# Kernel tuning notes

Measured on AMD Instinct MI355X. Metric: run time of the kernel, lower is better.

The kernel has to match this reference:

```python
import jax, jax.numpy as jnp
import numpy as np

N_NODES = 50000
N_EDGES = 800000
H = 128
D = 128
N_LAYERS = 4
N_GRAPHS = 128
NODE_VOCAB = 32
EDGE_VOCAB = 8
BN_EPS = 1e-5


def _bn(h, g, b):
    # BatchNorm1d, training-mode statistics (biased variance), as in the torch module
    m = h.mean(axis=0)
    v = ((h - m) ** 2).mean(axis=0)
    return (h - m) * jax.lax.rsqrt(v + BN_EPS) * g + b


def _gine(x, src, dst, e, eps_l):
    # GINEConv: message = ReLU(x_src + edge_attr), sum-aggregate at dst
    msg = jax.nn.relu(x[src] + e)                      # [E, H]
    aggr = jax.ops.segment_sum(msg, dst, num_segments=N_NODES)
    return (1.0 + eps_l) * x + aggr


def _forward(x_ids, edge_index, batch, edge_attr,
             node_emb, edge_emb, eps,
             init_W1, init_b1, init_g1, init_be1, init_W2, init_b2, init_g2, init_be2,
             mp_W1, mp_g1, mp_be1, mp_W2, mp_g2, mp_be2,
             l1_W1, l1_g1, l1_b1, l1_W2, l1_g2, l1_b2,
             l2_W1, l2_g1, l2_b1, l2_W2, l2_g2, l2_b2,
             fin_W):
    src, dst = edge_index[0], edge_index[1]
    x = node_emb[x_ids]                                # [N, H]
    e = edge_emb[edge_attr]                            # [E, H]
    # initialization conv (Linear layers WITH bias)
    h = _gine(x, src, dst, e, eps[0])
    h = jax.nn.relu(_bn(h @ init_W1 + init_b1, init_g1, init_be1))
    x = jax.nn.relu(_bn(h @ init_W2 + init_b2, init_g2, init_be2))
    # message-passing layers (Linear layers WITHOUT bias)
    for i in range(N_LAYERS):
        h = _gine(x, src, dst, e, eps[1 + i])
        h = jax.nn.relu(_bn(h @ mp_W1[i], mp_g1[i], mp_be1[i]))
        x = jax.nn.relu(_bn(h @ mp_W2[i], mp_g2[i], mp_be2[i]))
    # readout: global_add_pool
    g = jax.ops.segment_sum(x, batch, num_segments=N_GRAPHS)   # [G, H]
    # lin1 (outer F.relu is idempotent; dropout = identity in eval)
    h = jax.nn.relu(_bn(g @ l1_W1, l1_g1, l1_b1))
    h = jax.nn.relu(_bn(h @ l1_W2, l1_g2, l1_b2))
    # lin2
    h = jax.nn.relu(_bn(h @ l2_W1, l2_g1, l2_b1))
    h = jax.nn.relu(_bn(h @ l2_W2, l2_g2, l2_b2))
    return h @ fin_W                                   # [G, 1]


def setup_inputs() -> dict:
    key = jax.random.key(0)
    ks = jax.random.split(key, 20)
    s = 1.0 / np.sqrt(H)
    rn = lambda k, shp, sc: jax.random.normal(k, shp, dtype=jnp.float32) * sc
    return {
        "x_ids": jax.random.randint(ks[0], (N_NODES,), 0, NODE_VOCAB),
        "edge_index": jax.random.randint(ks[1], (2, N_EDGES), 0, N_NODES),
        "batch": jnp.sort(jax.random.randint(ks[2], (N_NODES,), 0, N_GRAPHS)),
        "edge_attr": jax.random.randint(ks[14], (N_EDGES,), 0, EDGE_VOCAB),
        "node_emb": rn(ks[3], (NODE_VOCAB, H), 0.05),
        "edge_emb": rn(ks[4], (EDGE_VOCAB, H), 0.05),
        "eps": jnp.zeros((N_LAYERS + 1,), jnp.float32),
        "init_W1": rn(ks[5], (H, D), s), "init_b1": jnp.zeros((D,)),
        "init_g1": jnp.ones((D,)), "init_be1": jnp.zeros((D,)),
        "init_W2": rn(ks[6], (D, H), s), "init_b2": jnp.zeros((H,)),
        "init_g2": jnp.ones((H,)), "init_be2": jnp.zeros((H,)),
        "mp_W1": rn(ks[7], (N_LAYERS, H, D), s),
        "mp_g1": jnp.ones((N_LAYERS, D)), "mp_be1": jnp.zeros((N_LAYERS, D)),
        "mp_W2": rn(ks[8], (N_LAYERS, D, H), s),
        "mp_g2": jnp.ones((N_LAYERS, H)), "mp_be2": jnp.zeros((N_LAYERS, H)),
        "l1_W1": rn(ks[9], (H, D), s), "l1_g1": jnp.ones((D,)), "l1_b1": jnp.zeros((D,)),
        "l1_W2": rn(ks[10], (D, D), s), "l1_g2": jnp.ones((D,)), "l1_b2": jnp.zeros((D,)),
        "l2_W1": rn(ks[11], (D, D), s), "l2_g1": jnp.ones((D,)), "l2_b1": jnp.zeros((D,)),
        "l2_W2": rn(ks[12], (D, H), s), "l2_g2": jnp.ones((H,)), "l2_b2": jnp.zeros((H,)),
        "fin_W": rn(ks[13], (H, 1), s),
    }


def reference(x_ids, edge_index, batch, edge_attr,
              node_emb, edge_emb, eps,
              init_W1, init_b1, init_g1, init_be1, init_W2, init_b2, init_g2, init_be2,
              mp_W1, mp_g1, mp_be1, mp_W2, mp_g2, mp_be2,
              l1_W1, l1_g1, l1_b1, l1_W2, l1_g2, l1_b2,
              l2_W1, l2_g1, l2_b1, l2_W2, l2_g2, l2_b2,
              fin_W):
    return _forward(x_ids, edge_index, batch, edge_attr,
                    node_emb, edge_emb, eps,
                    init_W1, init_b1, init_g1, init_be1, init_W2, init_b2, init_g2, init_be2,
                    mp_W1, mp_g1, mp_be1, mp_W2, mp_g2, mp_be2,
                    l1_W1, l1_g1, l1_b1, l1_W2, l1_g2, l1_b2,
                    l2_W1, l2_g1, l2_b1, l2_W2, l2_g2, l2_b2,
                    fin_W)
```

## Files before the change

### kernel.cpp

```cpp
#include <hip/hip_runtime.h>

#define NN 50000
#define NE 800000
#define NG 128
#define HD 128
#define NL 4
#define BN_EPS 1e-5f
#define REP 32
#define WP 136
#define NB 392
#define EPB 4096

typedef __attribute__((ext_vector_type(8))) short bf16x8;
typedef __attribute__((ext_vector_type(4))) float f32x4;

__device__ __forceinline__ unsigned short f2bf(float f) {
    unsigned u = __float_as_uint(f);
    u += 0x7FFFu + ((u >> 16) & 1u);
    return (unsigned short)(u >> 16);
}
__device__ __forceinline__ float bfval(unsigned short h) { return __uint_as_float((unsigned)h << 16); }
__device__ __forceinline__ float bflo(unsigned u) { return __uint_as_float(u << 16); }
__device__ __forceinline__ float bfhi(unsigned u) { return __uint_as_float(u & 0xFFFF0000u); }

__device__ __forceinline__ void split2(float a, float b, unsigned& hi, unsigned& lo) {
    unsigned ua = __float_as_uint(a), ub = __float_as_uint(b);
    hi = (ua >> 16) | (ub & 0xFFFF0000u);
    float ra = a - __uint_as_float(ua & 0xFFFF0000u);
    float rb = b - __uint_as_float(ub & 0xFFFF0000u);
    lo = (unsigned)f2bf(ra) | ((unsigned)f2bf(rb) << 16);
}
__device__ __forceinline__ unsigned pack2(float a, float b) {
    return (unsigned)f2bf(a) | ((unsigned)f2bf(b) << 16);
}

__device__ __forceinline__ void bn_pre(const float* SQbase,
                                       const float* gam, const float* bet,
                                       float inv_cnt, int t, float* scs, float* shs) {
    if (gam == nullptr) { scs[t] = 1.f; shs[t] = 0.f; return; }
    float s = 0.f, q = 0.f;
#pragma unroll
    for (int r = 0; r < REP; r++) {
        s += SQbase[r * 256 + t];
        q += SQbase[r * 256 + 128 + t];
    }
    float m = s * inv_cnt;
    float var = fmaxf(fmaf(q, inv_cnt, -m * m), 0.f);
    float inv = rsqrtf(var + BN_EPS);
    float sc = gam[t] * inv;
    scs[t] = sc;
    shs[t] = fmaf(-m, sc, bet[t]);
}

__global__ __launch_bounds__(256) void setup_kernel(const int* __restrict__ ids,
                                                    const float* __restrict__ emb,
                                                    unsigned short* __restrict__ Yb,
                                                    const float* __restrict__ iw1,
                                                    const float* __restrict__ iw2,
                                                    const float* __restrict__ mw1,
                                                    const float* __restrict__ mw2,
                                                    const float* __restrict__ hw1,
                                                    const float* __restrict__ hw2,
                                                    const float* __restrict__ hw3,
                                                    const float* __restrict__ hw4,
                                                    unsigned short* __restrict__ Wh,
                                                    unsigned short* __restrict__ Wl,
                                                    const int* __restrict__ dst,
                                                    int* __restrict__ deg) {
    int b = blockIdx.x, t = threadIdx.x;
    if (b < 3125) {
        int i = b * 256 + t;
        if (i < NN * 16) {
            int node = i >> 4, g = i & 15;
            int id = ids[node];
            const float* p = emb + (size_t)id * HD + 8 * g;
            float4 a = *(const float4*)p;
            float4 bb = *(const float4*)(p + 4);
            uint4 o;
            o.x = pack2(a.x, a.y); o.y = pack2(a.z, a.w);
            o.z = pack2(bb.x, bb.y); o.w = pack2(bb.z, bb.w);
            *(uint4*)(Yb + (size_t)node * HD + 8 * g) = o;
        }
    } else if (b < 4021) {
        int i = (b - 3125) * 256 + t;
        if (i < 229376) {
            int seg = i >> 14, loc = i & 16383;
            float v;
            if (seg == 0)       v = iw1[loc];
            else if (seg == 1)  v = iw2[loc];
            else if (seg < 6)   v = mw1[(seg - 2) * 16384 + loc];
            else if (seg < 10)  v = mw2[(seg - 6) * 16384 + loc];
            else if (seg == 10) v = hw1[loc];
            else if (seg == 11) v = hw2[loc];
            else if (seg == 12) v = hw3[loc];
            else                v = hw4[loc];
            int k = loc >> 7, n = loc & 127;
            unsigned short h = f2bf(v);
            float r = v - bfval(h);
            Wh[seg * 16384 + n * 128 + k] = h;
            Wl[seg * 16384 + n * 128 + k] = f2bf(r);
        }
    } else {
        int e = (b - 4021) * 256 + t;
        if (e < NE) atomicAdd(&deg[dst[e]], 1);
    }
}

__global__ __launch_bounds__(256) void ybn_kernel(const float* __restrict__ X,
                                                  const float* __restrict__ SQin,
                                                  const float* __restrict__ gam,
                                                  const float* __restrict__ bet,
                                                  unsigned short* __restrict__ Yb) {
    __shared__ float scs[HD], shs[HD];
    int t = threadIdx.x;
    if (t < HD) bn_pre(SQin, gam, bet, 1.f / NN, t, scs, shs);
    __syncthreads();
    int c8 = (t & 15) * 8;
    float4 s0 = *(const float4*)&scs[c8], s1 = *(const float4*)&scs[c8 + 4];
    float4 h0 = *(const float4*)&shs[c8], h1 = *(const float4*)&shs[c8 + 4];
#pragma unroll
    for (int ch = 0; ch < 4; ch++) {
        int row = blockIdx.x * 64 + ch * 16 + (t >> 4);
        if (row < NN) {
            const float* p = X + (size_t)row * HD + c8;
            float4 v0 = *(const float4*)p;
            float4 v1 = *(const float4*)(p + 4);
            float f0 = fmaxf(fmaf(v0.x, s0.x, h0.x), 0.f), f1 = fmaxf(fmaf(v0.y, s0.y, h0.y), 0.f);
            float f2 = fmaxf(fmaf(v0.z, s0.z, h0.z), 0.f), f3 = fmaxf(fmaf(v0.w, s0.w, h0.w), 0.f);
            float f4 = fmaxf(fmaf(v1.x, s1.x, h1.x), 0.f), f5 = fmaxf(fmaf(v1.y, s1.y, h1.y), 0.f);
            float f6 = fmaxf(fmaf(v1.z, s1.z, h1.z), 0.f), f7 = fmaxf(fmaf(v1.w, s1.w, h1.w), 0.f);
            uint4 o;
            o.x = pack2(f0, f1); o.y = pack2(f2, f3);
            o.z = pack2(f4, f5); o.w = pack2(f6, f7);
            *(uint4*)(Yb + (size_t)row * HD + c8) = o;
        }
    }
}

__global__ __launch_bounds__(1024) void scan1_kernel(const int* __restrict__ deg,
                                                     int* __restrict__ rowptr,
                                                     int* __restrict__ blockSum) {
    __shared__ int s[1024];
    int b = blockIdx.x, t = threadIdx.x;
    int i = b * 1024 + t;
    int v = (i < NN) ? deg[i] : 0;
    s[t] = v;
    __syncthreads();
    for (int off = 1; off < 1024; off <<= 1) {
        int u = (t >= off) ? s[t - off] : 0;
        __syncthreads();
        s[t] += u;
        __syncthreads();
    }
    if (i < NN) rowptr[i] = s[t] - v;
    if (t == 1023) blockSum[b] = s[1023];
}

__global__ __launch_bounds__(1024) void scan3_kernel(int* __restrict__ rowptr,
                                                     int* __restrict__ cursor,
                                                     const int* __restrict__ blockSum,
                                                     int* __restrict__ bucketCursor,
                                                     int nblocks) {
    __shared__ int sOff, sTot;
    int b = blockIdx.x, t = threadIdx.x;
    if (t < 64) {
        int orig = (t < nblocks) ? blockSum[t] : 0;
        int v = orig;
        for (int off = 1; off < 64; off <<= 1) {
            int u = __shfl_up(v, off, 64);
            if (t >= off) v += u;
        }
        if (t == b) sOff = v - orig;
        if (t == nblocks - 1) sTot = v;
    }
    __syncthreads();
    int i = b * 1024 + t;
    if (i < NN) {
        int r = rowptr[i] + sOff;
        rowptr[i] = r;
        cursor[i] = r;
        if ((i & 127) == 0) bucketCursor[i >> 7] = r;
    }
    if (b == nblocks - 1 && t == 0) rowptr[NN] = sTot;
}

__global__ __launch_bounds__(256) void bin_kernel(const int* __restrict__ src,
                                                  const int* __restrict__ dst,
                                                  const int* __restrict__ attr,
                                                  int* __restrict__ bucketCursor,
                                                  uint2* __restrict__ ebuf) {
    __shared__ int cnt[512];
    __shared__ int sc[512], sc2[512];
    __shared__ int base[512];
    __shared__ int garr[NB];
    __shared__ int wof[NB];
    __shared__ uint2 stage[EPB];
    int t = threadIdx.x;
    int e0 = blockIdx.x * EPB;
    for (int i = t; i < 512; i += 256) cnt[i] = 0;
    __syncthreads();
    int myb[16]; unsigned myv[16]; int myd[16];
#pragma unroll
    for (int j = 0; j < 16; j++) {
        int e = e0 + t + j * 256;
        if (e < NE) {
            int d = dst[e];
            myd[j] = d;
            myv[j] = (unsigned)src[e] | ((unsigned)attr[e] << 16);
            myb[j] = d >> 7;
            atomicAdd(&cnt[myb[j]], 1);
        } else myb[j] = -1;
    }
    __syncthreads();
    for (int k = t; k < 512; k += 256) sc[k] = cnt[k];
    __syncthreads();
    int* sp = sc; int* dp = sc2;
    for (int off = 1; off < 512; off <<= 1) {
        for (int k = t; k < 512; k += 256) dp[k] = sp[k] + (k >= off ? sp[k - off] : 0);
        __syncthreads();
        int* tmp = sp; sp = dp; dp = tmp;
    }
    for (int k = t; k < 512; k += 256) base[k] = sp[k] - cnt[k];
    int total = sp[511];
    __syncthreads();
    for (int b = t; b < NB; b += 256) {
        wof[b] = 0;
        if (cnt[b] > 0) garr[b] = atomicAdd(&bucketCursor[b], cnt[b]);
    }
    __syncthreads();
#pragma unroll
    for (int j = 0; j < 16; j++) {
        if (myb[j] >= 0) {
            int slot = base[myb[j]] + atomicAdd(&wof[myb[j]], 1);
            stage[slot] = make_uint2(myv[j], (unsigned)myd[j]);
        }
    }
    __syncthreads();
    for (int i = t; i < total; i += 256) {
        uint2 u = stage[i];
        int b = (int)(u.y >> 7);
        ebuf[garr[b] + (i - base[b])] = u;
    }
}

__global__ __launch_bounds__(256) void place_kernel(const uint2* __restrict__ ebuf,
                                                    const int* __restrict__ rowptr,
                                                    int* __restrict__ cursor,
                                                    unsigned* __restrict__ csr) {
    int b = blockIdx.x;
    int n0 = b * 128;
    int n1 = n0 + 128; if (n1 > NN) n1 = NN;
    int es = rowptr[n0], ee = rowptr[n1];
    for (int i = es + threadIdx.x; i < ee; i += 256) {
        uint2 u = ebuf[i];
        int pos = atomicAdd(&cursor[u.y], 1);
        csr[pos] = u.x;
    }
}

__device__ __forceinline__ void gine_acc(const unsigned short* __restrict__ Yb,
                                         const float* __restrict__ elds,
                                         unsigned p, int cq, float mask, float* a) {
    uint4 q = *(const uint4*)(Yb + (size_t)(p & 0xFFFFu) * HD + 8 * cq);
    const float* ep = elds + (p >> 16) * HD + 8 * cq;
    float4 e0 = *(const float4*)ep;
    float4 e1 = *(const float4*)(ep + 4);
    a[0] += mask * fmaxf(bflo(q.x) + e0.x, 0.f);
    a[1] += mask * fmaxf(bfhi(q.x) + e0.y, 0.f);
    a[2] += mask * fmaxf(bflo(q.y) + e0.z, 0.f);
    a[3] += mask * fmaxf(bfhi(q.y) + e0.w, 0.f);
    a[4] += mask * fmaxf(bflo(q.z) + e1.x, 0.f);
    a[5] += mask * fmaxf(bfhi(q.z) + e1.y, 0.f);
    a[6] += mask * fmaxf(bflo(q.w) + e1.z, 0.f);
    a[7] += mask * fmaxf(bfhi(q.w) + e1.w, 0.f);
}

__global__ __launch_bounds__(256) void conv_kernel(const unsigned short* __restrict__ Yb,
                                                   const int* __restrict__ rowptr,
                                                   const unsigned* __restrict__ csr,
                                                   const float* __restrict__ edge_emb,
                                                   const float* __restrict__ eps, int layer,
                                                   unsigned short* __restrict__ Ah,
                                                   unsigned short* __restrict__ Al) {
    __shared__ float elds[8 * HD];
    int t = threadIdx.x;
    ((float4*)elds)[t] = ((const float4*)edge_emb)[t];
    __syncthreads();
    int wave = t >> 6, lane = t & 63;
    int node = blockIdx.x * 4 + wave;
    if (node >= NN) return;
    int sub = lane >> 4, cq = lane & 15;
    int lo = rowptr[node], hi = rowptr[node + 1];
    float a[8];
#pragma unroll
    for (int i = 0; i < 8; i++) a[i] = 0.f;
    for (int base = lo; base < hi; base += 64) {
        unsigned pl = 0;
        int cnt = hi - base; if (cnt > 64) cnt = 64;
        if (base + lane < hi) pl = csr[base + lane];
        int j = 0;
        for (; j + 16 <= cnt; j += 16) {
            unsigned pa = __shfl(pl, j + sub, 64);
            unsigned pb = __shfl(pl, j + 4 + sub, 64);
            unsigned pc = __shfl(pl, j + 8 + sub, 64);
            unsigned pd = __shfl(pl, j + 12 + sub, 64);
            gine_acc(Yb, elds, pa, cq, 1.f, a);
            gine_acc(Yb, elds, pb, cq, 1.f, a);
            gine_acc(Yb, elds, pc, cq, 1.f, a);
            gine_acc(Yb, elds, pd, cq, 1.f, a);
        }
        for (; j + 8 <= cnt; j += 8) {
            unsigned pa = __shfl(pl, j + sub, 64);
            unsigned pb = __shfl(pl, j + 4 + sub, 64);
            gine_acc(Yb, elds, pa, cq, 1.f, a);
            gine_acc(Yb, elds, pb, cq, 1.f, a);
        }
        for (; j < cnt; j += 4) {
            int je = j + sub;
            bool val = (je < cnt);
            unsigned p = __shfl(pl, val ? je : j, 64);
            gine_acc(Yb, elds, p, cq, val ? 1.f : 0.f, a);
        }
    }
#pragma unroll
    for (int i = 0; i < 8; i++) {
        a[i] += __shfl_xor(a[i], 16, 64);
        a[i] += __shfl_xor(a[i], 32, 64);
    }
    if (sub == 0) {
        float g = 1.f + eps[layer];
        uint4 q = *(const uint4*)(Yb + (size_t)node * HD + 8 * cq);
        float o0 = fmaf(g, bflo(q.x), a[0]), o1 = fmaf(g, bfhi(q.x), a[1]);
        float o2 = fmaf(g, bflo(q.y), a[2]), o3 = fmaf(g, bfhi(q.y), a[3]);
        float o4 = fmaf(g, bflo(q.z), a[4]), o5 = fmaf(g, bfhi(q.z), a[5]);
        float o6 = fmaf(g, bflo(q.w), a[6]), o7 = fmaf(g, bfhi(q.w), a[7]);
        uint4 H, L;
        split2(o0, o1, H.x, L.x);
        split2(o2, o3, H.y, L.y);
        split2(o4, o5, H.z, L.z);
        split2(o6, o7, H.w, L.w);
        *(uint4*)(Ah + (size_t)node * HD + 8 * cq) = H;
        *(uint4*)(Al + (size_t)node * HD + 8 * cq) = L;
    }
}

__global__ __launch_bounds__(512) void mm_mfma_pre(const unsigned short* __restrict__ Ah,
                                                   const unsigned short* __restrict__ Al,
                                                   const unsigned short* __restrict__ Wh,
                                                   const unsigned short* __restrict__ Wl,
                                                   const float* __restrict__ bias,
                                                   float* __restrict__ out,
                                                   float* __restrict__ SQout) {
    __shared__ unsigned short WhS[128 * WP];
    __shared__ unsigned short WlS[128 * WP];
    int t = threadIdx.x;
    int rowblk = blockIdx.x;
#pragma unroll
    for (int i = 0; i < 4; i++) {
        int idx = t + i * 512;
        int col = idx >> 4, kk = (idx & 15) * 8;
        *(uint4*)(WhS + col * WP + kk) = *(const uint4*)(Wh + (size_t)col * HD + kk);
        *(uint4*)(WlS + col * WP + kk) = *(const uint4*)(Wl + (size_t)col * HD + kk);
    }
    __syncthreads();
    int w = t >> 6, lane = t & 63;
    int quad = lane >> 4, nl = lane & 15;
    int row0 = rowblk * 128 + w * 16;
    int rA0 = row0 + nl;
    bool ok0 = rA0 < NN;
    f32x4 acc[8];
#pragma unroll
    for (int i = 0; i < 8; i++) acc[i] = (f32x4){0.f, 0.f, 0.f, 0.f};
#pragma unroll
    for (int kc = 0; kc < 4; kc++) {
        int k0 = kc * 32 + quad * 8;
        bf16x8 a0h = ok0 ? *(const bf16x8*)(Ah + (size_t)rA0 * HD + k0) : (bf16x8)0;
        bf16x8 a0l = ok0 ? *(const bf16x8*)(Al + (size_t)rA0 * HD + k0) : (bf16x8)0;
#pragma unroll
        for (int c = 0; c < 8; c++) {
            int wof = (c * 16 + nl) * WP + k0;
            bf16x8 bh = *(const bf16x8*)(WhS + wof);
            bf16x8 bl = *(const bf16x8*)(WlS + wof);
            acc[c] = __builtin_amdgcn_mfma_f32_16x16x32_bf16(a0h, bh, acc[c], 0, 0, 0);
            acc[c] = __builtin_amdgcn_mfma_f32_16x16x32_bf16(a0l, bh, acc[c], 0, 0, 0);
            acc[c] = __builtin_amdgcn_mfma_f32_16x16x32_bf16(a0h, bl, acc[c], 0, 0, 0);
        }
    }
    int rep = (blockIdx.x & (REP - 1)) * 256;
    int baserow = row0 + quad * 4;
    if (rowblk * 128 + 128 <= NN) {
#pragma unroll
        for (int c = 0; c < 8; c++) {
            int col = c * 16 + nl;
            float bv = bias ? bias[col] : 0.f;
            f32x4 v = acc[c];
            float s = 0.f, qq = 0.f;
#pragma unroll
            for (int r = 0; r < 4; r++) {
                float val = v[r] + bv;
                out[(size_t)(baserow + r) * HD + col] = val;
                s += val;
                qq += val * val;
            }
            s += __shfl_xor(s, 16, 64);  s += __shfl_xor(s, 32, 64);
            qq += __shfl_xor(qq, 16, 64); qq += __shfl_xor(qq, 32, 64);
            if (quad == 0) {
                atomicAdd(&SQout[rep + col], s);
                atomicAdd(&SQout[rep + 128 + col], qq);
            }
        }
    } else {
#pragma unroll
        for (int c = 0; c < 8; c++) {
            int col = c * 16 + nl;
            float bv = bias ? bias[col] : 0.f;
            f32x4 v = acc[c];
            float s = 0.f, qq = 0.f;
#pragma unroll
            for (int r = 0; r < 4; r++) {
                int grow = baserow + r;
                float val = v[r] + bv;
                if (grow < NN) {
                    out[(size_t)grow * HD + col] = val;
                    s += val;
                    qq += val * val;
                }
            }
            s += __shfl_xor(s, 16, 64);  s += __shfl_xor(s, 32, 64);
            qq += __shfl_xor(qq, 16, 64); qq += __shfl_xor(qq, 32, 64);
            if (quad == 0) {
                atomicAdd(&SQout[rep + col], s);
                atomicAdd(&SQout[rep + 128 + col], qq);
            }
        }
    }
}

__global__ __launch_bounds__(512) void mm_mfma_act(const float* __restrict__ A,
                                                   const unsigned short* __restrict__ Wh,
                                                   const unsigned short* __restrict__ Wl,
                                                   const float* __restrict__ bias,
                                                   const float* __restrict__ SQin,
                                                   const float* __restrict__ gam,
                                                   const float* __restrict__ bet,
                                                   float* __restrict__ out,
                                                   float* __restrict__ SQout) {
    __shared__ unsigned short WhS[128 * WP];
    __shared__ unsigned short WlS[128 * WP];
    __shared__ float scs[HD], shs[HD];
    int t = threadIdx.x;
    int rowblk = blockIdx.x;
    if (t < HD) bn_pre(SQin, gam, bet, 1.f / NN, t, scs, shs);
#pragma unroll
    for (int i = 0; i < 4; i++) {
        int idx = t + i * 512;
        int col = idx >> 4, kk = (idx & 15) * 8;
        *(uint4*)(WhS + col * WP + kk) = *(const uint4*)(Wh + (size_t)col * HD + kk);
        *(uint4*)(WlS + col * WP + kk) = *(const uint4*)(Wl + (size_t)col * HD + kk);
    }
    __syncthreads();
    int w = t >> 6, lane = t & 63;
    int quad = lane >> 4, nl = lane & 15;
    int row0 = rowblk * 128 + w * 16;
    int rA0 = row0 + nl;
    bool ok0 = rA0 < NN;
    f32x4 acc[8];
#pragma unroll
    for (int i = 0; i < 8; i++) acc[i] = (f32x4){0.f, 0.f, 0.f, 0.f};
#pragma unroll
    for (int kc = 0; kc < 4; kc++) {
        int k0 = kc * 32 + quad * 8;
        float4 s0 = *(const float4*)&scs[k0], s1 = *(const float4*)&scs[k0 + 4];
        float4 t0 = *(const float4*)&shs[k0], t1 = *(const float4*)&shs[k0 + 4];
        bf16x8 a0h, a0l;
        {
            float4 v0 = ok0 ? *(const float4*)(A + (size_t)rA0 * HD + k0) : make_float4(0, 0, 0, 0);
            float4 v1 = ok0 ? *(const float4*)(A + (size_t)rA0 * HD + k0 + 4) : make_float4(0, 0, 0, 0);
            float f0 = fmaxf(fmaf(v0.x, s0.x, t0.x), 0.f), f1 = fmaxf(fmaf(v0.y, s0.y, t0.y), 0.f);
            float f2 = fmaxf(fmaf(v0.z, s0.z, t0.z), 0.f), f3 = fmaxf(fmaf(v0.w, s0.w, t0.w), 0.f);
            float f4 = fmaxf(fmaf(v1.x, s1.x, t1.x), 0.f), f5 = fmaxf(fmaf(v1.y, s1.y, t1.y), 0.f);
            float f6 = fmaxf(fmaf(v1.z, s1.z, t1.z), 0.f), f7 = fmaxf(fmaf(v1.w, s1.w, t1.w), 0.f);
            if (!ok0) { f0 = f1 = f2 = f3 = f4 = f5 = f6 = f7 = 0.f; }
            unsigned h0, h1, h2, h3, l0, l1, l2, l3;
            split2(f0, f1, h0, l0); split2(f2, f3, h1, l1);
            split2(f4, f5, h2, l2); split2(f6, f7, h3, l3);
            a0h = __builtin_bit_cast(bf16x8, make_uint4(h0, h1, h2, h3));
            a0l = __builtin_bit_cast(bf16x8, make_uint4(l0, l1, l2, l3));
        }
#pragma unroll
        for (int c = 0; c < 8; c++) {
            int wof = (c * 16 + nl) * WP + k0;
            bf16x8 bh = *(const bf16x8*)(WhS + wof);
            bf16x8 bl = *(const bf16x8*)(WlS + wof);
            acc[c] = __builtin_amdgcn_mfma_f32_16x16x32_bf16(a0h, bh, acc[c], 0, 0, 0);
            acc[c] = __builtin_amdgcn_mfma_f32_16x16x32_bf16(a0l, bh, acc[c], 0, 0, 0);
            acc[c] = __builtin_amdgcn_mfma_f32_16x16x32_bf16(a0h, bl, acc[c], 0, 0, 0);
        }
    }
    int rep = (blockIdx.x & (REP - 1)) * 256;
    int baserow = row0 + quad * 4;
    if (rowblk * 128 + 128 <= NN) {
#pragma unroll
        for (int c = 0; c < 8; c++) {
            int col = c * 16 + nl;
            float bv = bias ? bias[col] : 0.f;
            f32x4 v = acc[c];
            float s = 0.f, qq = 0.f;
#pragma unroll
            for (int r = 0; r < 4; r++) {
                float val = v[r] + bv;
                out[(size_t)(baserow + r) * HD + col] = val;
                s += val;
                qq += val * val;
            }
            s += __shfl_xor(s, 16, 64);  s += __shfl_xor(s, 32, 64);
            qq += __shfl_xor(qq, 16, 64); qq += __shfl_xor(qq, 32, 64);
            if (quad == 0) {
                atomicAdd(&SQout[rep + col], s);
                atomicAdd(&SQout[rep + 128 + col], qq);
            }
        }
    } else {
#pragma unroll
        for (int c = 0; c < 8; c++) {
            int col = c * 16 + nl;
            float bv = bias ? bias[col] : 0.f;
            f32x4 v = acc[c];
            float s = 0.f, qq = 0.f;
#pragma unroll
            for (int r = 0; r < 4; r++) {
                int grow = baserow + r;
                float val = v[r] + bv;
                if (grow < NN) {
                    out[(size_t)grow * HD + col] = val;
                    s += val;
                    qq += val * val;
                }
            }
            s += __shfl_xor(s, 16, 64);  s += __shfl_xor(s, 32, 64);
            qq += __shfl_xor(qq, 16, 64); qq += __shfl_xor(qq, 32, 64);
            if (quad == 0) {
                atomicAdd(&SQout[rep + col], s);
                atomicAdd(&SQout[rep + 128 + col], qq);
            }
        }
    }
}

__global__ __launch_bounds__(256) void readout_kernel(const float* __restrict__ x,
                                                      const int* __restrict__ batch,
                                                      const float* __restrict__ SQin,
                                                      const float* __restrict__ gam,
                                                      const float* __restrict__ bet,
                                                      float* __restrict__ gout) {
    __shared__ int bat[256];
    __shared__ float scs[HD], shs[HD];
    int t = threadIdx.x;
    int rq = t >> 5, cq = t & 31;
    int r0 = blockIdx.x * 256;
    int i = r0 + t;
    bat[t] = (i < NN) ? batch[i] : -1;
    if (t < HD) bn_pre(SQin, gam, bet, 1.f / NN, t, scs, shs);
    __syncthreads();
    float4 s4 = *(const float4*)&scs[4 * cq];
    float4 h4 = *(const float4*)&shs[4 * cq];
    float4 acc = make_float4(0.f, 0.f, 0.f, 0.f);
    int gcur = -1;
    for (int j = rq; j < 256; j += 8) {
        int r = r0 + j;
        if (r >= NN) break;
        int g = bat[j];
        if (g != gcur) {
            if (gcur >= 0) {
                atomicAdd(&gout[(size_t)gcur * HD + 4 * cq + 0], acc.x);
                atomicAdd(&gout[(size_t)gcur * HD + 4 * cq + 1], acc.y);
                atomicAdd(&gout[(size_t)gcur * HD + 4 * cq + 2], acc.z);
                atomicAdd(&gout[(size_t)gcur * HD + 4 * cq + 3], acc.w);
            }
            acc = make_float4(0.f, 0.f, 0.f, 0.f);
            gcur = g;
        }
        float4 v = *(const float4*)(x + (size_t)r * HD + 4 * cq);
        acc.x += fmaxf(fmaf(v.x, s4.x, h4.x), 0.f);
        acc.y += fmaxf(fmaf(v.y, s4.y, h4.y), 0.f);
        acc.z += fmaxf(fmaf(v.z, s4.z, h4.z), 0.f);
        acc.w += fmaxf(fmaf(v.w, s4.w, h4.w), 0.f);
    }
    if (gcur >= 0) {
        atomicAdd(&gout[(size_t)gcur * HD + 4 * cq + 0], acc.x);
        atomicAdd(&gout[(size_t)gcur * HD + 4 * cq + 1], acc.y);
        atomicAdd(&gout[(size_t)gcur * HD + 4 * cq + 2], acc.z);
        atomicAdd(&gout[(size_t)gcur * HD + 4 * cq + 3], acc.w);
    }
}

__global__ __launch_bounds__(1024) void head_fused(const float* __restrict__ Gp,
                                                   const unsigned short* __restrict__ Whd,
                                                   const unsigned short* __restrict__ Wld,
                                                   const float* __restrict__ g0,
                                                   const float* __restrict__ b0,
                                                   const float* __restrict__ g1,
                                                   const float* __restrict__ b1,
                                                   const float* __restrict__ g2,
                                                   const float* __restrict__ b2,
                                                   const float* __restrict__ g3,
                                                   const float* __restrict__ b3,
                                                   const float* __restrict__ finW,
                                                   float* __restrict__ out) {
    const int AP = 132;
    __shared__ float A_lds[128 * AP];
    __shared__ unsigned short WhS[128 * WP];
    __shared__ unsigned short WlS[128 * WP];
    __shared__ float colS[HD], colQ[HD], scs[HD], shs[HD];
    int t = threadIdx.x;
    if (t < HD) { colS[t] = 0.f; colQ[t] = 0.f; scs[t] = 1.f; shs[t] = 0.f; }
#pragma unroll
    for (int i = 0; i < 4; i++) {
        int idx = t + i * 1024;
        int r = idx >> 5, cq = (idx & 31) * 4;
        *(float4*)&A_lds[r * AP + cq] = *(const float4*)(Gp + (size_t)r * HD + cq);
    }
    int sc_ = t >> 4;
    int sk_ = (t & 15) * 8;
    const float* gs[4] = {g0, g1, g2, g3};
    const float* bs[4] = {b0, b1, b2, b3};
    uint4 ph0 = *(const uint4*)(Whd + (size_t)sc_ * HD + sk_);
    uint4 ph1 = *(const uint4*)(Whd + (size_t)(sc_ + 64) * HD + sk_);
    uint4 pl0 = *(const uint4*)(Wld + (size_t)sc_ * HD + sk_);
    uint4 pl1 = *(const uint4*)(Wld + (size_t)(sc_ + 64) * HD + sk_);
    int w = t >> 6, lane = t & 63;
    int quad = lane >> 4, nl = lane & 15;
    int row0 = (w >> 2) * 32, col0 = (w & 3) * 32;
#pragma unroll
    for (int s = 0; s < 4; s++) {
        *(uint4*)(WhS + sc_ * WP + sk_) = ph0;
        *(uint4*)(WhS + (sc_ + 64) * WP + sk_) = ph1;
        *(uint4*)(WlS + sc_ * WP + sk_) = pl0;
        *(uint4*)(WlS + (sc_ + 64) * WP + sk_) = pl1;
        __syncthreads();
        if (s < 3) {
            const unsigned short* nh = Whd + (size_t)(s + 1) * 16384;
            const unsigned short* nl2 = Wld + (size_t)(s + 1) * 16384;
            ph0 = *(const uint4*)(nh + (size_t)sc_ * HD + sk_);
            ph1 = *(const uint4*)(nh + (size_t)(sc_ + 64) * HD + sk_);
            pl0 = *(const uint4*)(nl2 + (size_t)sc_ * HD + sk_);
            pl1 = *(const uint4*)(nl2 + (size_t)(sc_ + 64) * HD + sk_);
        }
        f32x4 acc[4];
#pragma unroll
        for (int i = 0; i < 4; i++) acc[i] = (f32x4){0.f, 0.f, 0.f, 0.f};
#pragma unroll
        for (int kc = 0; kc < 4; kc++) {
            int k0 = kc * 32 + quad * 8;
            float4 s0 = *(const float4*)&scs[k0], s1 = *(const float4*)&scs[k0 + 4];
            float4 t0 = *(const float4*)&shs[k0], t1 = *(const float4*)&shs[k0 + 4];
            bf16x8 a0h, a0l, a1h, a1l;
            {
                const float* ap = &A_lds[(row0 + nl) * AP + k0];
                float4 v0 = *(const float4*)ap;
                float4 v1 = *(const float4*)(ap + 4);
                float f0 = fmaxf(fmaf(v0.x, s0.x, t0.x), 0.f), f1 = fmaxf(fmaf(v0.y, s0.y, t0.y), 0.f);
                float f2 = fmaxf(fmaf(v0.z, s0.z, t0.z), 0.f), f3 = fmaxf(fmaf(v0.w, s0.w, t0.w), 0.f);
                float f4 = fmaxf(fmaf(v1.x, s1.x, t1.x), 0.f), f5 = fmaxf(fmaf(v1.y, s1.y, t1.y), 0.f);
                float f6 = fmaxf(fmaf(v1.z, s1.z, t1.z), 0.f), f7 = fmaxf(fmaf(v1.w, s1.w, t1.w), 0.f);
                unsigned h0, h1, h2, h3, l0, l1, l2, l3;
                split2(f0, f1, h0, l0); split2(f2, f3, h1, l1);
                split2(f4, f5, h2, l2); split2(f6, f7, h3, l3);
                a0h = __builtin_bit_cast(bf16x8, make_uint4(h0, h1, h2, h3));
                a0l = __builtin_bit_cast(bf16x8, make_uint4(l0, l1, l2, l3));
            }
            {
                const float* ap = &A_lds[(row0 + 16 + nl) * AP + k0];
                float4 v0 = *(const float4*)ap;
                float4 v1 = *(const float4*)(ap + 4);
                float f0 = fmaxf(fmaf(v0.x, s0.x, t0.x), 0.f), f1 = fmaxf(fmaf(v0.y, s0.y, t0.y), 0.f);
                float f2 = fmaxf(fmaf(v0.z, s0.z, t0.z), 0.f), f3 = fmaxf(fmaf(v0.w, s0.w, t0.w), 0.f);
                float f4 = fmaxf(fmaf(v1.x, s1.x, t1.x), 0.f), f5 = fmaxf(fmaf(v1.y, s1.y, t1.y), 0.f);
                float f6 = fmaxf(fmaf(v1.z, s1.z, t1.z), 0.f), f7 = fmaxf(fmaf(v1.w, s1.w, t1.w), 0.f);
                unsigned h0, h1, h2, h3, l0, l1, l2, l3;
                split2(f0, f1, h0, l0); split2(f2, f3, h1, l1);
                split2(f4, f5, h2, l2); split2(f6, f7, h3, l3);
                a1h = __builtin_bit_cast(bf16x8, make_uint4(h0, h1, h2, h3));
                a1l = __builtin_bit_cast(bf16x8, make_uint4(l0, l1, l2, l3));
            }
#pragma unroll
            for (int cc = 0; cc < 2; cc++) {
                int wof = (col0 + cc * 16 + nl) * WP + k0;
                bf16x8 bh = *(const bf16x8*)(WhS + wof);
                bf16x8 bl = *(const bf16x8*)(WlS + wof);
                acc[cc] = __builtin_amdgcn_mfma_f32_16x16x32_bf16(a0h, bh, acc[cc], 0, 0, 0);
                acc[cc] = __builtin_amdgcn_mfma_f32_16x16x32_bf16(a0l, bh, acc[cc], 0, 0, 0);
                acc[cc] = __builtin_amdgcn_mfma_f32_16x16x32_bf16(a0h, bl, acc[cc], 0, 0, 0);
                acc[2 + cc] = __builtin_amdgcn_mfma_f32_16x16x32_bf16(a1h, bh, acc[2 + cc], 0, 0, 0);
                acc[2 + cc] = __builtin_amdgcn_mfma_f32_16x16x32_bf16(a1l, bh, acc[2 + cc], 0, 0, 0);
                acc[2 + cc] = __builtin_amdgcn_mfma_f32_16x16x32_bf16(a1h, bl, acc[2 + cc], 0, 0, 0);
            }
        }
        __syncthreads();
#pragma unroll
        for (int h = 0; h < 2; h++) {
            int baserow = row0 + h * 16 + quad * 4;
#pragma unroll
            for (int cc = 0; cc < 2; cc++) {
                int col = col0 + cc * 16 + nl;
                f32x4 v = acc[h * 2 + cc];
                float ss = 0.f, qq = 0.f;
#pragma unroll
                for (int r = 0; r < 4; r++) {
                    float val = v[r];
                    A_lds[(baserow + r) * AP + col] = val;
                    ss += val;
                    qq += val * val;
                }
                ss += __shfl_xor(ss, 16, 64);  ss += __shfl_xor(ss, 32, 64);
                qq += __shfl_xor(qq, 16, 64);  qq += __shfl_xor(qq, 32, 64);
                if (quad == 0) {
                    atomicAdd(&colS[col], ss);
                    atomicAdd(&colQ[col], qq);
                }
            }
        }
        __syncthreads();
        if (t < HD) {
            float m = colS[t] * (1.f / NG);
            float var = fmaxf(fmaf(colQ[t], 1.f / NG, -m * m), 0.f);
            float inv = rsqrtf(var + BN_EPS);
            float sc = gs[s][t] * inv;
            scs[t] = sc;
            shs[t] = fmaf(-m, sc, bs[s][t]);
            colS[t] = 0.f;
            colQ[t] = 0.f;
        }
        __syncthreads();
    }
    int r = t >> 3, g = t & 7;
    float ssum = 0.f;
#pragma unroll
    for (int j = 0; j < 16; j++) {
        int c = g * 16 + j;
        float v = fmaxf(fmaf(A_lds[r * AP + c], scs[c], shs[c]), 0.f);
        ssum += v * finW[c];
    }
    ssum += __shfl_xor(ssum, 1, 64);
    ssum += __shfl_xor(ssum, 2, 64);
    ssum += __shfl_xor(ssum, 4, 64);
    if (g == 0) out[r] = ssum;
}

extern "C" void kernel_launch(void* const* d_in, const int* in_sizes, int n_in,
                              void* d_out, int out_size, void* d_ws, size_t ws_size,
                              hipStream_t stream) {
    const int* x_ids = (const int*)d_in[0];
    const int* edge_index = (const int*)d_in[1];
    const int* batch = (const int*)d_in[2];
    const int* edge_attr = (const int*)d_in[3];
    const float* node_emb = (const float*)d_in[4];
    const float* edge_emb = (const float*)d_in[5];
    const float* eps = (const float*)d_in[6];
    const float* init_W1 = (const float*)d_in[7];
    const float* init_b1 = (const float*)d_in[8];
    const float* init_g1 = (const float*)d_in[9];
    const float* init_be1 = (const float*)d_in[10];
    const float* init_W2 = (const float*)d_in[11];
    const float* init_b2 = (const float*)d_in[12];
    const float* init_g2 = (const float*)d_in[13];
    const float* init_be2 = (const float*)d_in[14];
    const float* mp_W1 = (const float*)d_in[15];
    const float* mp_g1 = (const float*)d_in[16];
    const float* mp_be1 = (const float*)d_in[17];
    const float* mp_W2 = (const float*)d_in[18];
    const float* mp_g2 = (const float*)d_in[19];
    const float* mp_be2 = (const float*)d_in[20];
    const float* l1_W1 = (const float*)d_in[21];
    const float* l1_g1 = (const float*)d_in[22];
    const float* l1_b1 = (const float*)d_in[23];
    const float* l1_W2 = (const float*)d_in[24];
    const float* l1_g2 = (const float*)d_in[25];
    const float* l1_b2 = (const float*)d_in[26];
    const float* l2_W1 = (const float*)d_in[27];
    const float* l2_g1 = (const float*)d_in[28];
    const float* l2_b1 = (const float*)d_in[29];
    const float* l2_W2 = (const float*)d_in[30];
    const float* l2_g2 = (const float*)d_in[31];
    const float* l2_b2 = (const float*)d_in[32];
    const float* fin_W = (const float*)d_in[33];

    const int* e_src = edge_index;
    const int* e_dst = edge_index + NE;

    const size_t STG = (size_t)REP * 256;
    float* ws = (float*)d_ws;
    float* X = ws;
    float* Bbuf = X + (size_t)NN * HD;
    unsigned short* Yb = (unsigned short*)Bbuf;
    unsigned short* Ah = (unsigned short*)(Bbuf + (size_t)NN * HD);
    unsigned short* Al = Ah + (size_t)NN * HD;
    float* SQ = (float*)(Al + (size_t)NN * HD);
    float* Gp = SQ + 14 * STG;
    int* deg = (int*)(Gp + NG * HD);
    float* Hp = (float*)(deg + 50048);
    float* Hp2 = Hp + NG * HD;
    int* rowptr = (int*)(Hp2 + NG * HD);
    int* cursor = rowptr + 50048;
    int* blockSum = cursor + 50048;
    int* blockOff = blockSum + 64;
    int* bucketCursor = blockOff + 64;
    unsigned* csr = (unsigned*)(bucketCursor + NB);
    unsigned short* Wh = (unsigned short*)(csr + NE);
    unsigned short* Wl = Wh + 229376;
    uint2* ebuf = (uint2*)(Wl + 229376);
    (void)Hp; (void)Hp2; (void)blockOff;

    const size_t zero_bytes = (14 * STG + NG * HD) * sizeof(float) + 50048 * sizeof(int);
    hipMemsetAsync(SQ, 0, zero_bytes, stream);

    const int SCAN_BLOCKS = (NN + 1023) / 1024;
    setup_kernel<<<7146, 256, 0, stream>>>(x_ids, node_emb, Yb, init_W1, init_W2, mp_W1,
                                           mp_W2, l1_W1, l1_W2, l2_W1, l2_W2,
                                           Wh, Wl, e_dst, deg);
    scan1_kernel<<<SCAN_BLOCKS, 1024, 0, stream>>>(deg, rowptr, blockSum);
    scan3_kernel<<<SCAN_BLOCKS, 1024, 0, stream>>>(rowptr, cursor, blockSum, bucketCursor,
                                                   SCAN_BLOCKS);
    bin_kernel<<<(NE + EPB - 1) / EPB, 256, 0, stream>>>(e_src, e_dst, edge_attr,
                                                         bucketCursor, ebuf);
    place_kernel<<<(NN + 127) / 128, 256, 0, stream>>>(ebuf, rowptr, cursor, csr);

    const int mfma_grid = (NN + 127) / 128;
    const int ybn_grid = (NN + 63) / 64;
    for (int i = 0; i <= NL; i++) {
        const unsigned short* Wh1 = Wh + (size_t)(i == 0 ? 0 : 2 + (i - 1)) * 16384;
        const unsigned short* Wl1 = Wl + (size_t)(i == 0 ? 0 : 2 + (i - 1)) * 16384;
        const unsigned short* Wh2 = Wh + (size_t)(i == 0 ? 1 : 6 + (i - 1)) * 16384;
        const unsigned short* Wl2 = Wl + (size_t)(i == 0 ? 1 : 6 + (i - 1)) * 16384;
        const float* b1 = (i == 0) ? init_b1 : nullptr;
        const float* b2 = (i == 0) ? init_b2 : nullptr;
        const float* g1 = (i == 0) ? init_g1 : mp_g1 + (size_t)(i - 1) * HD;
        const float* be1 = (i == 0) ? init_be1 : mp_be1 + (size_t)(i - 1) * HD;
        const float* gp = (i == 1) ? init_g2 : mp_g2 + (size_t)(i - 2) * HD;
        const float* bp = (i == 1) ? init_be2 : mp_be2 + (size_t)(i - 2) * HD;
        float* Sprev = SQ + (size_t)(2 * i - 1) * STG;
        float* S1 = SQ + (size_t)(2 * i) * STG;
        float* S2 = SQ + (size_t)(2 * i + 1) * STG;

        if (i > 0) ybn_kernel<<<ybn_grid, 256, 0, stream>>>(X, Sprev, gp, bp, Yb);
        conv_kernel<<<(NN + 3) / 4, 256, 0, stream>>>(Yb, rowptr, csr, edge_emb, eps, i, Ah, Al);
        mm_mfma_pre<<<mfma_grid, 512, 0, stream>>>(Ah, Al, Wh1, Wl1, b1, Bbuf, S1);
        mm_mfma_act<<<mfma_grid, 512, 0, stream>>>(Bbuf, Wh2, Wl2, b2, S1, g1, be1, X, S2);
    }

    float* S9 = SQ + 9 * STG;
    readout_kernel<<<(NN + 255) / 256, 256, 0, stream>>>(
        X, batch, S9, mp_g2 + 3 * HD, mp_be2 + 3 * HD, Gp);

    head_fused<<<1, 1024, 0, stream>>>(Gp, Wh + (size_t)10 * 16384, Wl + (size_t)10 * 16384,
                                       l1_g1, l1_b1, l1_g2, l1_b2,
                                       l2_g1, l2_b1, l2_g2, l2_b2,
                                       fin_W, (float*)d_out);
}
```

Before: 675.7 us.

## Fuse two MFMA GEMM kernels with an in-kernel grid barrier for BN stats

Merges the two per-layer MFMA matmul kernels into one persistent launch. A global atomic-counter barrier waits for all blocks' first-GEMM BatchNorm statistics before the second GEMM runs. This removes one kernel launch per layer and keeps the block's rows hot in cache between the GEMMs. It relies on all ~391 blocks being co-resident (launch_bounds 512,4) to avoid deadlock, and adds spin-wait overhead. The barrier counters sit inside the memset-zeroed deg region.

```diff
diff --git a/kernel.cpp b/kernel.cpp
--- a/kernel.cpp
+++ b/kernel.cpp
@@ -344,23 +344,32 @@
     }
 }
 
-__global__ __launch_bounds__(512) void mm_mfma_pre(const unsigned short* __restrict__ Ah,
+__global__ __launch_bounds__(512, 4) void mm_fused(const unsigned short* __restrict__ Ah,
                                                    const unsigned short* __restrict__ Al,
-                                                   const unsigned short* __restrict__ Wh,
-                                                   const unsigned short* __restrict__ Wl,
-                                                   const float* __restrict__ bias,
-                                                   float* __restrict__ out,
-                                                   float* __restrict__ SQout) {
+                                                   const unsigned short* __restrict__ Wh1,
+                                                   const unsigned short* __restrict__ Wl1,
+                                                   const float* __restrict__ bias1,
+                                                   const unsigned short* __restrict__ Wh2,
+                                                   const unsigned short* __restrict__ Wl2,
+                                                   const float* __restrict__ bias2,
+                                                   const float* __restrict__ gam,
+                                                   const float* __restrict__ bet,
+                                                   float* __restrict__ Bbuf,
+                                                   float* __restrict__ S1,
+                                                   float* __restrict__ X,
+                                                   float* __restrict__ S2,
+                                                   int* __restrict__ barCnt, int nblk) {
     __shared__ unsigned short WhS[128 * WP];
     __shared__ unsigned short WlS[128 * WP];
+    __shared__ float scs[HD], shs[HD];
     int t = threadIdx.x;
     int rowblk = blockIdx.x;
 #pragma unroll
     for (int i = 0; i < 4; i++) {
         int idx = t + i * 512;
         int col = idx >> 4, kk = (idx & 15) * 8;
-        *(uint4*)(WhS + col * WP + kk) = *(const uint4*)(Wh + (size_t)col * HD + kk);
-        *(uint4*)(WlS + col * WP + kk) = *(const uint4*)(Wl + (size_t)col * HD + kk);
+        *(uint4*)(WhS + col * WP + kk) = *(const uint4*)(Wh1 + (size_t)col * HD + kk);
+        *(uint4*)(WlS + col * WP + kk) = *(const uint4*)(Wl1 + (size_t)col * HD + kk);
     }
     __syncthreads();
     int w = t >> 6, lane = t & 63;
@@ -368,180 +377,170 @@
     int row0 = rowblk * 128 + w * 16;
     int rA0 = row0 + nl;
     bool ok0 = rA0 < NN;
-    f32x4 acc[8];
-#pragma unroll
-    for (int i = 0; i < 8; i++) acc[i] = (f32x4){0.f, 0.f, 0.f, 0.f};
-#pragma unroll
-    for (int kc = 0; kc < 4; kc++) {
-        int k0 = kc * 32 + quad * 8;
-        bf16x8 a0h = ok0 ? *(const bf16x8*)(Ah + (size_t)rA0 * HD + k0) : (bf16x8)0;
-        bf16x8 a0l = ok0 ? *(const bf16x8*)(Al + (size_t)rA0 * HD + k0) : (bf16x8)0;
-#pragma unroll
-        for (int c = 0; c < 8; c++) {
-            int wof = (c * 16 + nl) * WP + k0;
-            bf16x8 bh = *(const bf16x8*)(WhS + wof);
-            bf16x8 bl = *(const bf16x8*)(WlS + wof);
-            acc[c] = __builtin_amdgcn_mfma_f32_16x16x32_bf16(a0h, bh, acc[c], 0, 0, 0);
-            acc[c] = __builtin_amdgcn_mfma_f32_16x16x32_bf16(a0l, bh, acc[c], 0, 0, 0);
-            acc[c] = __builtin_amdgcn_mfma_f32_16x16x32_bf16(a0h, bl, acc[c], 0, 0, 0);
-        }
-    }
-    int rep = (blockIdx.x & (REP - 1)) * 256;
+    bool fullblk = (rowblk * 128 + 128 <= NN);
+    int rep = (rowblk & (REP - 1)) * 256;
     int baserow = row0 + quad * 4;
-    if (rowblk * 128 + 128 <= NN) {
-#pragma unroll
-        for (int c = 0; c < 8; c++) {
-            int col = c * 16 + nl;
-            float bv = bias ? bias[col] : 0.f;
-            f32x4 v = acc[c];
-            float s = 0.f, qq = 0.f;
-#pragma unroll
-            for (int r = 0; r < 4; r++) {
-                float val = v[r] + bv;
-                out[(size_t)(baserow + r) * HD + col] = val;
-                s += val;
-                qq += val * val;
-            }
-            s += __shfl_xor(s, 16, 64);  s += __shfl_xor(s, 32, 64);
-            qq += __shfl_xor(qq, 16, 64); qq += __shfl_xor(qq, 32, 64);
-            if (quad == 0) {
-                atomicAdd(&SQout[rep + col], s);
-                atomicAdd(&SQout[rep + 128 + col], qq);
-            }
-        }
-    } else {
-#pragma unroll
-        for (int c = 0; c < 8; c++) {
-            int col = c * 16 + nl;
-            float bv = bias ? bias[col] : 0.f;
-            f32x4 v = acc[c];
-            float s = 0.f, qq = 0.f;
-#pragma unroll
-            for (int r = 0; r < 4; r++) {
-                int grow = baserow + r;
-                float val = v[r] + bv;
-                if (grow < NN) {
-                    out[(size_t)grow * HD + col] = val;
+    {
+        f32x4 acc[8];
+#pragma unroll
+        for (int i = 0; i < 8; i++) acc[i] = (f32x4){0.f, 0.f, 0.f, 0.f};
+#pragma unroll
+        for (int kc = 0; kc < 4; kc++) {
+            int k0 = kc * 32 + quad * 8;
+            bf16x8 a0h = ok0 ? *(const bf16x8*)(Ah + (size_t)rA0 * HD + k0) : (bf16x8)0;
+            bf16x8 a0l = ok0 ? *(const bf16x8*)(Al + (size_t)rA0 * HD + k0) : (bf16x8)0;
+#pragma unroll
+            for (int c = 0; c < 8; c++) {
+                int wof = (c * 16 + nl) * WP + k0;
+                bf16x8 bh = *(const bf16x8*)(WhS + wof);
+                bf16x8 bl = *(const bf16x8*)(WlS + wof);
+                acc[c] = __builtin_amdgcn_mfma_f32_16x16x32_bf16(a0h, bh, acc[c], 0, 0, 0);
+                acc[c] = __builtin_amdgcn_mfma_f32_16x16x32_bf16(a0l, bh, acc[c], 0, 0, 0);
+                acc[c] = __builtin_amdgcn_mfma_f32_16x16x32_bf16(a0h, bl, acc[c], 0, 0, 0);
+            }
+        }
+        if (fullblk) {
+#pragma unroll
+            for (int c = 0; c < 8; c++) {
+                int col = c * 16 + nl;
+                float bv = bias1 ? bias1[col] : 0.f;
+                f32x4 v = acc[c];
+                float s = 0.f, qq = 0.f;
+#pragma unroll
+                for (int r = 0; r < 4; r++) {
+                    float val = v[r] + bv;
+                    Bbuf[(size_t)(baserow + r) * HD + col] = val;
                     s += val;
                     qq += val * val;
                 }
-            }
-            s += __shfl_xor(s, 16, 64);  s += __shfl_xor(s, 32, 64);
-            qq += __shfl_xor(qq, 16, 64); qq += __shfl_xor(qq, 32, 64);
-            if (quad == 0) {
-                atomicAdd(&SQout[rep + col], s);
-                atomicAdd(&SQout[rep + 128 + col], qq);
-            }
-        }
-    }
-}
-
-__global__ __launch_bounds__(512) void mm_mfma_act(const float* __restrict__ A,
-                                                   const unsigned short* __restrict__ Wh,
-                                                   const unsigned short* __restrict__ Wl,
-                                                   const float* __restrict__ bias,
-                                                   const float* __restrict__ SQin,
-                                                   const float* __restrict__ gam,
-                                                   const float* __restrict__ bet,
-                                                   float* __restrict__ out,
-                                                   float* __restrict__ SQout) {
-    __shared__ unsigned short WhS[128 * WP];
-    __shared__ unsigned short WlS[128 * WP];
-    __shared__ float scs[HD], shs[HD];
-    int t = threadIdx.x;
-    int rowblk = blockIdx.x;
-    if (t < HD) bn_pre(SQin, gam, bet, 1.f / NN, t, scs, shs);
+                s += __shfl_xor(s, 16, 64);  s += __shfl_xor(s, 32, 64);
+                qq += __shfl_xor(qq, 16, 64); qq += __shfl_xor(qq, 32, 64);
+                if (quad == 0) {
+                    atomicAdd(&S1[rep + col], s);
+                    atomicAdd(&S1[rep + 128 + col], qq);
+                }
+            }
+        } else {
+#pragma unroll
+            for (int c = 0; c < 8; c++) {
+                int col = c * 16 + nl;
+                float bv = bias1 ? bias1[col] : 0.f;
+                f32x4 v = acc[c];
+                float s = 0.f, qq = 0.f;
+#pragma unroll
+                for (int r = 0; r < 4; r++) {
+                    int grow = baserow + r;
+                    float val = v[r] + bv;
+                    if (grow < NN) {
+                        Bbuf[(size_t)grow * HD + col] = val;
+                        s += val;
+                        qq += val * val;
+                    }
+                }
+                s += __shfl_xor(s, 16, 64);  s += __shfl_xor(s, 32, 64);
+                qq += __shfl_xor(qq, 16, 64); qq += __shfl_xor(qq, 32, 64);
+                if (quad == 0) {
+                    atomicAdd(&S1[rep + col], s);
+                    atomicAdd(&S1[rep + 128 + col], qq);
+                }
+            }
+        }
+    }
+    __syncthreads();
+    if (t == 0) {
+        __threadfence();
+        atomicAdd(barCnt, 1);
+        while (atomicAdd(barCnt, 0) < nblk) __builtin_amdgcn_s_sleep(2);
+        __threadfence();
+    }
+    __syncthreads();
+    if (t < HD) bn_pre(S1, gam, bet, 1.f / NN, t, scs, shs);
 #pragma unroll
     for (int i = 0; i < 4; i++) {
         int idx = t + i * 512;
         int col = idx >> 4, kk = (idx & 15) * 8;
-        *(uint4*)(WhS + col * WP + kk) = *(const uint4*)(Wh + (size_t)col * HD + kk);
-        *(uint4*)(WlS + col * WP + kk) = *(const uint4*)(Wl + (size_t)col * HD + kk);
-    }
-    __syncthreads();
-    int w = t >> 6, lane = t & 63;
-    int quad = lane >> 4, nl = lane & 15;
-    int row0 = rowblk * 128 + w * 16;
-    int rA0 = row0 + nl;
-    bool ok0 = rA0 < NN;
-    f32x4 acc[8];
-#pragma unroll
-    for (int i = 0; i < 8; i++) acc[i] = (f32x4){0.f, 0.f, 0.f, 0.f};
-#pragma unroll
-    for (int kc = 0; kc < 4; kc++) {
-        int k0 = kc * 32 + quad * 8;
-        float4 s0 = *(const float4*)&scs[k0], s1 = *(const float4*)&scs[k0 + 4];
-        float4 t0 = *(const float4*)&shs[k0], t1 = *(const float4*)&shs[k0 + 4];
-        bf16x8 a0h, a0l;
-        {
-            float4 v0 = ok0 ? *(const float4*)(A + (size_t)rA0 * HD + k0) : make_float4(0, 0, 0, 0);
-            float4 v1 = ok0 ? *(const float4*)(A + (size_t)rA0 * HD + k0 + 4) : make_float4(0, 0, 0, 0);
-            float f0 = fmaxf(fmaf(v0.x, s0.x, t0.x), 0.f), f1 = fmaxf(fmaf(v0.y, s0.y, t0.y), 0.f);
-            float f2 = fmaxf(fmaf(v0.z, s0.z, t0.z), 0.f), f3 = fmaxf(fmaf(v0.w, s0.w, t0.w), 0.f);
-            float f4 = fmaxf(fmaf(v1.x, s1.x, t1.x), 0.f), f5 = fmaxf(fmaf(v1.y, s1.y, t1.y), 0.f);
-            float f6 = fmaxf(fmaf(v1.z, s1.z, t1.z), 0.f), f7 = fmaxf(fmaf(v1.w, s1.w, t1.w), 0.f);
-            if (!ok0) { f0 = f1 = f2 = f3 = f4 = f5 = f6 = f7 = 0.f; }
-            unsigned h0, h1, h2, h3, l0, l1, l2, l3;
-            split2(f0, f1, h0, l0); split2(f2, f3, h1, l1);
-            split2(f4, f5, h2, l2); split2(f6, f7, h3, l3);
-            a0h = __builtin_bit_cast(bf16x8, make_uint4(h0, h1, h2, h3));
-            a0l = __builtin_bit_cast(bf16x8, make_uint4(l0, l1, l2, l3));
-        }
-#pragma unroll
-        for (int c = 0; c < 8; c++) {
-            int wof = (c * 16 + nl) * WP + k0;
-            bf16x8 bh = *(const bf16x8*)(WhS + wof);
-            bf16x8 bl = *(const bf16x8*)(WlS + wof);
-            acc[c] = __builtin_amdgcn_mfma_f32_16x16x32_bf16(a0h, bh, acc[c], 0, 0, 0);
-            acc[c] = __builtin_amdgcn_mfma_f32_16x16x32_bf16(a0l, bh, acc[c], 0, 0, 0);
-            acc[c] = __builtin_amdgcn_mfma_f32_16x16x32_bf16(a0h, bl, acc[c], 0, 0, 0);
-        }
-    }
-    int rep = (blockIdx.x & (REP - 1)) * 256;
-    int baserow = row0 + quad * 4;
-    if (rowblk * 128 + 128 <= NN) {
-#pragma unroll
-        for (int c = 0; c < 8; c++) {
-            int col = c * 16 + nl;
-            float bv = bias ? bias[col] : 0.f;
-            f32x4 v = acc[c];
-            float s = 0.f, qq = 0.f;
-#pragma unroll
-            for (int r = 0; r < 4; r++) {
-                float val = v[r] + bv;
-                out[(size_t)(baserow + r) * HD + col] = val;
-                s += val;
-                qq += val * val;
-            }
-            s += __shfl_xor(s, 16, 64);  s += __shfl_xor(s, 32, 64);
-            qq += __shfl_xor(qq, 16, 64); qq += __shfl_xor(qq, 32, 64);
-            if (quad == 0) {
-                atomicAdd(&SQout[rep + col], s);
-                atomicAdd(&SQout[rep + 128 + col], qq);
-            }
-        }
-    } else {
-#pragma unroll
-        for (int c = 0; c < 8; c++) {
-            int col = c * 16 + nl;
-            float bv = bias ? bias[col] : 0.f;
-            f32x4 v = acc[c];
-            float s = 0.f, qq = 0.f;
-#pragma unroll
-            for (int r = 0; r < 4; r++) {
-                int grow = baserow + r;
-                float val = v[r] + bv;
-                if (grow < NN) {
-                    out[(size_t)grow * HD + col] = val;
+        *(uint4*)(WhS + col * WP + kk) = *(const uint4*)(Wh2 + (size_t)col * HD + kk);
+        *(uint4*)(WlS + col * WP + kk) = *(const uint4*)(Wl2 + (size_t)col * HD + kk);
+    }
+    __syncthreads();
+    {
+        f32x4 acc[8];
+#pragma unroll
+        for (int i = 0; i < 8; i++) acc[i] = (f32x4){0.f, 0.f, 0.f, 0.f};
+#pragma unroll
+        for (int kc = 0; kc < 4; kc++) {
+            int k0 = kc * 32 + quad * 8;
+            float4 s0 = *(const float4*)&scs[k0], s1 = *(const float4*)&scs[k0 + 4];
+            float4 t0 = *(const float4*)&shs[k0], t1 = *(const float4*)&shs[k0 + 4];
+            bf16x8 a0h, a0l;
+            {
+                float4 v0 = ok0 ? *(const float4*)(Bbuf + (size_t)rA0 * HD + k0) : make_float4(0, 0, 0, 0);
+                float4 v1 = ok0 ? *(const float4*)(Bbuf + (size_t)rA0 * HD + k0 + 4) : make_float4(0, 0, 0, 0);
+                float f0 = fmaxf(fmaf(v0.x, s0.x, t0.x), 0.f), f1 = fmaxf(fmaf(v0.y, s0.y, t0.y), 0.f);
+                float f2 = fmaxf(fmaf(v0.z, s0.z, t0.z), 0.f), f3 = fmaxf(fmaf(v0.w, s0.w, t0.w), 0.f);
+                float f4 = fmaxf(fmaf(v1.x, s1.x, t1.x), 0.f), f5 = fmaxf(fmaf(v1.y, s1.y, t1.y), 0.f);
+                float f6 = fmaxf(fmaf(v1.z, s1.z, t1.z), 0.f), f7 = fmaxf(fmaf(v1.w, s1.w, t1.w), 0.f);
+                if (!ok0) { f0 = f1 = f2 = f3 = f4 = f5 = f6 = f7 = 0.f; }
+                unsigned h0, h1, h2, h3, l0, l1, l2, l3;
+                split2(f0, f1, h0, l0); split2(f2, f3, h1, l1);
+                split2(f4, f5, h2, l2); split2(f6, f7, h3, l3);
+                a0h = __builtin_bit_cast(bf16x8, make_uint4(h0, h1, h2, h3));
+                a0l = __builtin_bit_cast(bf16x8, make_uint4(l0, l1, l2, l3));
+            }
+#pragma unroll
+            for (int c = 0; c < 8; c++) {
+                int wof = (c * 16 + nl) * WP + k0;
+                bf16x8 bh = *(const bf16x8*)(WhS + wof);
+                bf16x8 bl = *(const bf16x8*)(WlS + wof);
+                acc[c] = __builtin_amdgcn_mfma_f32_16x16x32_bf16(a0h, bh, acc[c], 0, 0, 0);
+                acc[c] = __builtin_amdgcn_mfma_f32_16x16x32_bf16(a0l, bh, acc[c], 0, 0, 0);
+                acc[c] = __builtin_amdgcn_mfma_f32_16x16x32_bf16(a0h, bl, acc[c], 0, 0, 0);
+            }
+        }
+        if (fullblk) {
+#pragma unroll
+            for (int c = 0; c < 8; c++) {
+                int col = c * 16 + nl;
+                float bv = bias2 ? bias2[col] : 0.f;
+                f32x4 v = acc[c];
+                float s = 0.f, qq = 0.f;
+#pragma unroll
+                for (int r = 0; r < 4; r++) {
+                    float val = v[r] + bv;
+                    X[(size_t)(baserow + r) * HD + col] = val;
                     s += val;
                     qq += val * val;
                 }
-            }
-            s += __shfl_xor(s, 16, 64);  s += __shfl_xor(s, 32, 64);
-            qq += __shfl_xor(qq, 16, 64); qq += __shfl_xor(qq, 32, 64);
-            if (quad == 0) {
-                atomicAdd(&SQout[rep + col], s);
-                atomicAdd(&SQout[rep + 128 + col], qq);
+                s += __shfl_xor(s, 16, 64);  s += __shfl_xor(s, 32, 64);
+                qq += __shfl_xor(qq, 16, 64); qq += __shfl_xor(qq, 32, 64);
+                if (quad == 0) {
+                    atomicAdd(&S2[rep + col], s);
+                    atomicAdd(&S2[rep + 128 + col], qq);
+                }
+            }
+        } else {
+#pragma unroll
+            for (int c = 0; c < 8; c++) {
+                int col = c * 16 + nl;
+                float bv = bias2 ? bias2[col] : 0.f;
+                f32x4 v = acc[c];
+                float s = 0.f, qq = 0.f;
+#pragma unroll
+                for (int r = 0; r < 4; r++) {
+                    int grow = baserow + r;
+                    float val = v[r] + bv;
+                    if (grow < NN) {
+                        X[(size_t)grow * HD + col] = val;
+                        s += val;
+                        qq += val * val;
+                    }
+                }
+                s += __shfl_xor(s, 16, 64);  s += __shfl_xor(s, 32, 64);
+                qq += __shfl_xor(qq, 16, 64); qq += __shfl_xor(qq, 32, 64);
+                if (quad == 0) {
+                    atomicAdd(&S2[rep + col], s);
+                    atomicAdd(&S2[rep + 128 + col], qq);
+                }
             }
         }
     }
@@ -798,6 +797,7 @@
     float* SQ = (float*)(Al + (size_t)NN * HD);
     float* Gp = SQ + 14 * STG;
     int* deg = (int*)(Gp + NG * HD);
+    int* barCnt = deg + 50016;
     float* Hp = (float*)(deg + 50048);
     float* Hp2 = Hp + NG * HD;
     int* rowptr = (int*)(Hp2 + NG * HD);
@@ -844,8 +844,9 @@
 
         if (i > 0) ybn_kernel<<<ybn_grid, 256, 0, stream>>>(X, Sprev, gp, bp, Yb);
         conv_kernel<<<(NN + 3) / 4, 256, 0, stream>>>(Yb, rowptr, csr, edge_emb, eps, i, Ah, Al);
-        mm_mfma_pre<<<mfma_grid, 512, 0, stream>>>(Ah, Al, Wh1, Wl1, b1, Bbuf, S1);
-        mm_mfma_act<<<mfma_grid, 512, 0, stream>>>(Bbuf, Wh2, Wl2, b2, S1, g1, be1, X, S2);
+        mm_fused<<<mfma_grid, 512, 0, stream>>>(Ah, Al, Wh1, Wl1, b1, Wh2, Wl2, b2,
+                                                g1, be1, Bbuf, S1, X, S2,
+                                                barCnt + i, mfma_grid);
     }
 
     float* S9 = SQ + 9 * STG;
```

Measured after the change: 870.7 us. 28.9% more time.
